# Optimization experiments

Hardware: AMD Instinct MI355X
Metric: run time of the kernel (lower is better)

Reference implementation:

```python
import jax, jax.numpy as jnp
import numpy as np

B, S, E, H, DH, F = 4, 2048, 1024, 4, 256, 4096


def setup_inputs() -> dict:
    key = jax.random.key(0)
    ks = jax.random.split(key, 16)
    def w(k, shape):
        return jax.random.normal(k, shape, jnp.float32) * 0.02
    return {
        "inputs": jax.random.normal(ks[0], (B, S, E), jnp.float32),
        "context": jax.random.normal(ks[1], (B, S, E), jnp.float32),
        # self-attention (causal) per-head projections stacked over heads
        "Wk1": w(ks[2], (H, E, DH)), "bk1": jnp.zeros((H, DH), jnp.float32),
        "Wq1": w(ks[3], (H, E, DH)), "bq1": jnp.zeros((H, DH), jnp.float32),
        "Wv1": w(ks[4], (H, E, DH)), "bv1": jnp.zeros((H, DH), jnp.float32),
        "Wo1": w(ks[5], (E, E)), "bo1": jnp.zeros((E,), jnp.float32),
        # cross-attention (no mask)
        "Wk2": w(ks[6], (H, E, DH)), "bk2": jnp.zeros((H, DH), jnp.float32),
        "Wq2": w(ks[7], (H, E, DH)), "bq2": jnp.zeros((H, DH), jnp.float32),
        "Wv2": w(ks[8], (H, E, DH)), "bv2": jnp.zeros((H, DH), jnp.float32),
        "Wo2": w(ks[9], (E, E)), "bo2": jnp.zeros((E,), jnp.float32),
        "ln_g": jnp.ones((E,), jnp.float32), "ln_b": jnp.zeros((E,), jnp.float32),
        # FFN
        "W1": w(ks[10], (E, F)), "b1": jnp.zeros((F,), jnp.float32),
        "W2": w(ks[11], (F, E)), "b2": jnp.zeros((E,), jnp.float32),
    }


def _mha(kin, vin, qin, Wk, bk, Wq, bq, Wv, bv, Wo, bo, causal):
    # per-head Dense projections, batched over heads: [B,S,E] x [H,E,DH] -> [B,H,S,DH]
    K = jnp.einsum('bse,hed->bhsd', kin, Wk) + bk[None, :, None, :]
    Q = jnp.einsum('bse,hed->bhsd', qin, Wq) + bq[None, :, None, :]
    V = jnp.einsum('bse,hed->bhsd', vin, Wv) + bv[None, :, None, :]
    # NOTE: original divides by head_dim (K.get_shape()[2]), NOT sqrt(head_dim)
    scores = jnp.einsum('bhqd,bhkd->bhqk', Q, K) / K.shape[-1]
    if causal:
        sq, sk = scores.shape[-2], scores.shape[-1]
        mask = jnp.triu(jnp.full((sq, sk), -jnp.inf, scores.dtype), k=1)
        scores = scores + mask  # additive -inf strictly above the diagonal
    A = jax.nn.softmax(scores, axis=-1)
    # concat heads in order along the feature axis, then output Dense
    out = jnp.einsum('bhqk,bhkd->bqhd', A, V).reshape(qin.shape[0], qin.shape[1], -1)
    return out @ Wo + bo


def _ln(x, g, b):
    # keras LayerNormalization default epsilon = 1e-3
    m = x.mean(-1, keepdims=True)
    v = ((x - m) ** 2).mean(-1, keepdims=True)
    return (x - m) / jnp.sqrt(v + 1e-3) * g + b


def reference(inputs, context, Wk1, bk1, Wq1, bq1, Wv1, bv1, Wo1, bo1,
              Wk2, bk2, Wq2, bq2, Wv2, bv2, Wo2, bo2,
              ln_g, ln_b, W1, b1, W2, b2):
    # dropout layers are identity at inference
    a = _mha(inputs, inputs, inputs, Wk1, bk1, Wq1, bq1, Wv1, bv1, Wo1, bo1, True) + inputs
    a = _ln(a, ln_g, ln_b)
    # cross-attention: keys/values = context, queries = normalized self-attn output
    c = _mha(context, context, a, Wk2, bk2, Wq2, bq2, Wv2, bv2, Wo2, bo2, False) + a
    c = _ln(c, ln_g, ln_b)
    h = jax.nn.relu(c @ W1 + b1) @ W2 + b2 + c
    return jax.nn.relu(_ln(h, ln_g, ln_b))
```

## Files before the change

kernel.cpp:

```cpp
#include <hip/hip_runtime.h>

#define DEV __device__ __forceinline__

typedef unsigned short u16;
typedef __bf16 bf16x8 __attribute__((ext_vector_type(8)));
typedef bf16x8 __attribute__((may_alias)) bf16x8a;
typedef float f32x4 __attribute__((ext_vector_type(4)));
typedef float f32x16 __attribute__((ext_vector_type(16)));

constexpr int NB = 4, NS = 2048, NE = 1024, NH = 4, NDH = 256, NF = 4096;
constexpr int NR = NB * NS;

DEV u16 f2bf(float f) {
  unsigned u = __float_as_uint(f);
  u += 0x7fff + ((u >> 16) & 1);
  return (u16)(u >> 16);
}

DEV f32x4 mfma16(bf16x8 a, bf16x8 b, f32x4 c) {
  return __builtin_amdgcn_mfma_f32_16x16x32_bf16(a, b, c, 0, 0, 0);
}
DEV f32x16 mfma32(bf16x8 a, bf16x8 b, f32x16 c) {
  return __builtin_amdgcn_mfma_f32_32x32x16_bf16(a, b, c, 0, 0, 0);
}

DEV bf16x8 ldfrag(const u16* p) { return *(const bf16x8a*)p; }

DEV void gload_lds16(const void* g, void* l) {
  __builtin_amdgcn_global_load_lds(
      (const __attribute__((address_space(1))) void*)g,
      (__attribute__((address_space(3))) void*)l, 16, 0, 0);
}

DEV void blockbar() {
  asm volatile("" ::: "memory");
  __builtin_amdgcn_s_barrier();
  asm volatile("" ::: "memory");
}

DEV unsigned packbf(float a, float b) {
  union { __bf16 h[2]; unsigned u; } x;
  x.h[0] = (__bf16)a; x.h[1] = (__bf16)b;
  return x.u;
}

__global__ void cast_f32_bf16(const float* __restrict__ in, u16* __restrict__ out, int n4) {
  int i = blockIdx.x * 256 + threadIdx.x;
  if (i >= n4) return;
  float4 v = ((const float4*)in)[i];
  ushort4 o;
  o.x = f2bf(v.x); o.y = f2bf(v.y); o.z = f2bf(v.z); o.w = f2bf(v.w);
  ((ushort4*)out)[i] = o;
}

__global__ void transpose_cast(const float* __restrict__ in, u16* __restrict__ out, int R, int C) {
  __shared__ float t[32][33];
  size_t base = (size_t)blockIdx.z * R * C;
  int c0 = blockIdx.x * 32, r0 = blockIdx.y * 32;
  int x = threadIdx.x;
  for (int yy = threadIdx.y; yy < 32; yy += 8)
    t[yy][x] = in[base + (size_t)(r0 + yy) * C + c0 + x];
  __syncthreads();
  for (int yy = threadIdx.y; yy < 32; yy += 8)
    out[base + (size_t)(c0 + yy) * R + r0 + x] = f2bf(t[x][yy]);
}

__global__ void transpose_v(const u16* __restrict__ V, int vstride, u16* __restrict__ Vt) {
  __shared__ u16 t[32][34];
  int bh = blockIdx.z, b = bh >> 2, h = bh & (NH - 1);
  int s0 = blockIdx.x * 32, d0 = blockIdx.y * 32;
  int x = threadIdx.x;
  for (int yy = threadIdx.y; yy < 32; yy += 8)
    t[yy][x] = V[(size_t)(b * NS + s0 + yy) * vstride + h * NDH + d0 + x];
  __syncthreads();
  for (int yy = threadIdx.y; yy < 32; yy += 8)
    Vt[((size_t)bh * NDH + d0 + yy) * NS + s0 + x] = t[x][yy];
}

__global__ void copy_f32(const float* __restrict__ s, float* __restrict__ d, int n) {
  int i = blockIdx.x * 256 + threadIdx.x;
  if (i < n) d[i] = s[i];
}

template<int BN, int OUTF32, int RELU>
__global__ __launch_bounds__(512, 1)
void gemm8p(const u16* __restrict__ A, const u16* __restrict__ Bt,
            const float* __restrict__ bias, const float* __restrict__ res,
            float* __restrict__ outF, u16* __restrict__ outB,
            int M, int N, int K)
{
  constexpr int NFRAG = BN / 64;
  __shared__ __align__(16) u16 smem[32768 + 2 * BN * 64];

  int tid = threadIdx.x, w = tid >> 6, lane = tid & 63;
  int lr = lane & 15, lk = lane >> 4;
  int wm = w >> 2, wn = w & 3;

  int flat = blockIdx.y * gridDim.x + blockIdx.x;
  int cpx = (gridDim.x * gridDim.y) >> 3;
  int swz = (flat & 7) * cpx + (flat >> 3);
  int bx = swz % gridDim.x, by = swz / gridDim.x;
  int rowBlk = by * 256, colBlk = bx * BN;

  f32x4 acc[8][NFRAG];
#pragma unroll
  for (int f = 0; f < 8; f++)
#pragma unroll
    for (int n = 0; n < NFRAG; n++) acc[f][n] = (f32x4){0.f, 0.f, 0.f, 0.f};

  int srow = lane >> 3;
  int scol = ((lane & 7) ^ (srow & 7)) * 8;

  const u16* gA = A + (size_t)rowBlk * K;
  const u16* gB = Bt + (size_t)colBlk * K;

  auto stageA = [&](int t, int p, int h) {
#pragma unroll
    for (int j = 0; j < 2; j++) {
      int rbase = h * 128 + (w * 2 + j) * 8;
      gload_lds16(gA + (size_t)(rbase + srow) * K + t * 64 + scol,
                  &smem[(p * 256 + rbase) * 64]);
    }
  };
  auto stageB = [&](int t, int p, int h) {
#pragma unroll
    for (int j = 0; j < 2; j++) {
      int rbase = h * 128 + (w * 2 + j) * 8;
      gload_lds16(gB + (size_t)(rbase + srow) * K + t * 64 + scol,
                  &smem[32768 + (p * BN + rbase) * 64]);
    }
  };

  stageB(0, 0, 0);
  if (BN == 256) stageB(0, 0, 1);
  stageA(0, 0, 0);
  stageA(0, 0, 1);
  asm volatile("s_waitcnt vmcnt(0)" ::: "memory");
  blockbar();

  int NT = K >> 6;
  for (int t = 0; t < NT; t++) {
    int p = t & 1;
    bool pre = (t + 1 < NT);
    bf16x8 bf[NFRAG][2];
#pragma unroll
    for (int q = 0; q < 4; q++) {
      if (q == 0) {
#pragma unroll
        for (int n = 0; n < NFRAG; n++)
#pragma unroll
          for (int s = 0; s < 2; s++) {
            int rowB = wn * (BN >> 2) + n * 16 + lr;
            bf[n][s] = ldfrag(&smem[32768 + (p * BN + rowB) * 64 +
                                    (((s * 4 + lk) ^ (lr & 7)) * 8)]);
          }
      }
      bf16x8 af[2][2];
#pragma unroll
      for (int i = 0; i < 2; i++)
#pragma unroll
        for (int s = 0; s < 2; s++) {
          int rowA = wm * 128 + (q * 2 + i) * 16 + lr;
          af[i][s] = ldfrag(&smem[(p * 256 + rowA) * 64 +
                                  (((s * 4 + lk) ^ (lr & 7)) * 8)]);
        }
      if (pre) {
        if (BN == 256) {
          if (q == 0) { stageB(t + 1, p ^ 1, 0); stageB(t + 1, p ^ 1, 1); }
          else if (q == 1) stageA(t + 1, p ^ 1, 0);
          else if (q == 2) stageA(t + 1, p ^ 1, 1);
        } else {
          if (q == 0) stageB(t + 1, p ^ 1, 0);
          else if (q == 1) stageA(t + 1, p ^ 1, 0);
          else if (q == 2) stageA(t + 1, p ^ 1, 1);
        }
      }
      blockbar();
      asm volatile("s_waitcnt lgkmcnt(0)" ::: "memory");
      __builtin_amdgcn_s_setprio(1);
#pragma unroll
      for (int i = 0; i < 2; i++)
#pragma unroll
        for (int n = 0; n < NFRAG; n++)
#pragma unroll
          for (int s = 0; s < 2; s++)
            acc[q * 2 + i][n] = mfma16(af[i][s], bf[n][s], acc[q * 2 + i][n]);
      __builtin_amdgcn_s_setprio(0);
      if (q == 3) asm volatile("s_waitcnt vmcnt(0)" ::: "memory");
      blockbar();
    }
  }

  int orow0 = rowBlk + wm * 128;
  int ocol0 = colBlk + wn * (BN >> 2);
#pragma unroll
  for (int n = 0; n < NFRAG; n++) {
    int c = ocol0 + n * 16 + lr;
    float bv = bias[c];
#pragma unroll
    for (int f = 0; f < 8; f++) {
      int r0 = orow0 + f * 16 + lk * 4;
#pragma unroll
      for (int j = 0; j < 4; j++) {
        float v = acc[f][n][j] + bv;
        if (OUTF32) v += res[(size_t)(r0 + j) * N + c];
        if (RELU) v = fmaxf(v, 0.f);
        if (OUTF32) outF[(size_t)(r0 + j) * N + c] = v;
        else        outB[(size_t)(r0 + j) * N + c] = f2bf(v);
      }
    }
  }
}

template<int CAUSAL>
__global__ __launch_bounds__(512, 2)
void attn8w(const u16* __restrict__ Qp, int qstride,
            const u16* __restrict__ Kp, int kstride,
            const u16* __restrict__ Vt, u16* __restrict__ O)
{
  __shared__ __align__(16) u16 smem[65536];

  int bidx = blockIdx.x;
  int bh = bidx & 15;
  int qt = CAUSAL ? (15 - (bidx >> 4)) : (bidx >> 4);
  int b = bh >> 2, h = bh & 3;
  int tid = threadIdx.x, w = tid >> 6, lane = tid & 63;
  int L = lane & 31, hi = lane >> 5;
  int g = w >> 1, ks = w & 1;

  int qbase = qt * 128 + g * 32;

  const u16* qrow = Qp + (size_t)(b * NS + qbase + L) * qstride + h * NDH;
  bf16x8 qf[16];
#pragma unroll
  for (int s = 0; s < 16; s++) qf[s] = ldfrag(qrow + s * 16 + hi * 8);

  f32x16 oacc[8];
#pragma unroll
  for (int db = 0; db < 8; db++) oacc[db] = (f32x16){};
  float m = -1e30f, l = 0.f;

  int nkt = CAUSAL ? (2 * qt + 2) : (NS / 64);
  constexpr float SC = 1.0f / NDH;

  const u16* kbase = Kp + (size_t)(b * NS) * kstride + h * NDH;
  const u16* vbase = Vt + (size_t)bh * NDH * NS;

  auto stage = [&](int kt, int buf) {
#pragma unroll
    for (int ii = 0; ii < 4; ii++) {
      int gi = w * 4 + ii;
      int krow = 2 * gi + hi;
      int kcol = L ^ (krow & 31);
      gload_lds16(kbase + (size_t)(kt * 64 + krow) * kstride + kcol * 8,
                  &smem[buf * 16384 + gi * 512]);
      int vd = gi * 8 + (lane >> 3);
      int vg = (lane & 7) ^ (vd & 7);
      gload_lds16(vbase + (size_t)vd * NS + kt * 64 + vg * 8,
                  &smem[32768 + buf * 16384 + gi * 512]);
    }
  };

  stage(0, 0);

  for (int kt = 0; kt < nkt; kt++) {
    int buf = kt & 1;
    const u16* bK = &smem[buf * 16384];
    const u16* bV = &smem[32768 + buf * 16384];
    if (kt + 1 < nkt) {
      stage(kt + 1, buf ^ 1);
      asm volatile("s_waitcnt vmcnt(8)" ::: "memory");
    } else {
      asm volatile("s_waitcnt vmcnt(0)" ::: "memory");
    }
    blockbar();

    int ksub0 = kt * 64 + ks * 32;
    bool skip = CAUSAL && (ksub0 > qbase + 31);
    if (!skip) {
      bool domask = CAUSAL && (ksub0 + 31 > qbase);
      __builtin_amdgcn_s_setprio(1);
      f32x16 sa = (f32x16){};
#pragma unroll
      for (int s = 0; s < 16; s++) {
        int row = ks * 32 + L;
        bf16x8 kf = ldfrag(&bK[row * 256 + (((2 * s + hi) ^ L) & 31) * 8]);
        sa = mfma32(kf, qf[s], sa);
      }
      __builtin_amdgcn_s_setprio(0);

      float p[16];
      float tmax = -1e30f;
#pragma unroll
      for (int r = 0; r < 16; r++) {
        float v = sa[r] * SC;
        if (domask) {
          int key = ksub0 + (r & 3) + 8 * (r >> 2) + 4 * hi;
          if (key > qbase + L) v = -1e30f;
        }
        p[r] = v;
        tmax = fmaxf(tmax, v);
      }
      tmax = fmaxf(tmax, __shfl_xor(tmax, 32));

      float mn = m;
      if (!__all(tmax - m <= 5.0f)) {
        mn = fmaxf(m, tmax);
        float rs = __expf(m - mn);
        m = mn;
        l *= rs;
#pragma unroll
        for (int db = 0; db < 8; db++)
#pragma unroll
          for (int r = 0; r < 16; r++) oacc[db][r] *= rs;
      }
      float psum = 0.f;
#pragma unroll
      for (int r = 0; r < 16; r++) {
        p[r] = __expf(p[r] - mn);
        psum += p[r];
      }
      psum += __shfl_xor(psum, 32);
      l += psum;

      unsigned pk01 = packbf(p[0], p[1]),  pk23 = packbf(p[2], p[3]);
      unsigned pk45 = packbf(p[4], p[5]),  pk67 = packbf(p[6], p[7]);
      unsigned pk89 = packbf(p[8], p[9]),  pkab = packbf(p[10], p[11]);
      unsigned pkcd = packbf(p[12], p[13]), pkef = packbf(p[14], p[15]);
      unsigned s45 = (unsigned)__shfl_xor((int)pk45, 32);
      unsigned s67 = (unsigned)__shfl_xor((int)pk67, 32);
      unsigned s01 = (unsigned)__shfl_xor((int)pk01, 32);
      unsigned s23 = (unsigned)__shfl_xor((int)pk23, 32);
      unsigned scd = (unsigned)__shfl_xor((int)pkcd, 32);
      unsigned sef = (unsigned)__shfl_xor((int)pkef, 32);
      unsigned s89 = (unsigned)__shfl_xor((int)pk89, 32);
      unsigned sab = (unsigned)__shfl_xor((int)pkab, 32);
      union { unsigned u[4]; bf16x8 v; } fb0, fb1;
      fb0.u[0] = hi ? s45 : pk01;
      fb0.u[1] = hi ? s67 : pk23;
      fb0.u[2] = hi ? pk45 : s01;
      fb0.u[3] = hi ? pk67 : s23;
      fb1.u[0] = hi ? scd : pk89;
      fb1.u[1] = hi ? sef : pkab;
      fb1.u[2] = hi ? pkcd : s89;
      fb1.u[3] = hi ? pkef : sab;
      bf16x8 pb0 = fb0.v, pb1 = fb1.v;

      __builtin_amdgcn_s_setprio(1);
#pragma unroll
      for (int db = 0; db < 8; db++) {
        int vd = db * 32 + L;
        bf16x8 vf0 = ldfrag(&bV[vd * 64 + (((ks * 4 + hi) ^ (vd & 7)) & 7) * 8]);
        bf16x8 vf1 = ldfrag(&bV[vd * 64 + (((ks * 4 + 2 + hi) ^ (vd & 7)) & 7) * 8]);
        oacc[db] = mfma32(vf0, pb0, oacc[db]);
        oacc[db] = mfma32(vf1, pb1, oacc[db]);
      }
      __builtin_amdgcn_s_setprio(0);
    }
    blockbar();
  }

  float* fsm = (float*)smem;
  blockbar();
  if (hi == 0) { fsm[w * 64 + L * 2] = m; fsm[w * 64 + L * 2 + 1] = l; }
  blockbar();
  float mb = fsm[(w ^ 1) * 64 + L * 2];
  float lb = fsm[(w ^ 1) * 64 + L * 2 + 1];
  float M = fmaxf(m, mb);
  float eo = __expf(m - M);
  float lt = l * eo + lb * __expf(mb - M);
  blockbar();
  float* reg = fsm + g * 8192;
  if (w & 1) {
#pragma unroll
    for (int db = 0; db < 8; db++)
#pragma unroll
      for (int r = 0; r < 16; r++) {
        int d = db * 32 + (r & 3) + 8 * (r >> 2) + 4 * hi;
        reg[d * 32 + L] = oacc[db][r] * eo;
      }
  }
  blockbar();
  if (!(w & 1)) {
    float inv = 1.f / lt;
    size_t orow = (size_t)(b * NS + qbase + L) * NE + h * NDH;
#pragma unroll
    for (int db = 0; db < 8; db++) {
#pragma unroll
      for (int rq = 0; rq < 4; rq++) {
        int d0 = db * 32 + rq * 8 + hi * 4;
        float a0 = (oacc[db][rq * 4 + 0] * eo + reg[(d0 + 0) * 32 + L]) * inv;
        float a1 = (oacc[db][rq * 4 + 1] * eo + reg[(d0 + 1) * 32 + L]) * inv;
        float a2 = (oacc[db][rq * 4 + 2] * eo + reg[(d0 + 2) * 32 + L]) * inv;
        float a3 = (oacc[db][rq * 4 + 3] * eo + reg[(d0 + 3) * 32 + L]) * inv;
        uint2 wv;
        wv.x = packbf(a0, a1);
        wv.y = packbf(a2, a3);
        *(uint2*)&O[orow + d0] = wv;
      }
    }
  }
}

template<int RELU, int WBF>
__global__ __launch_bounds__(256)
void ln_kernel(const float* __restrict__ x, const float* __restrict__ g,
               const float* __restrict__ bb, float* __restrict__ outF,
               u16* __restrict__ outB)
{
  int row = blockIdx.x, tid = threadIdx.x;
  float4 v = ((const float4*)(x + (size_t)row * NE))[tid];
  float s = v.x + v.y + v.z + v.w;
  float s2 = v.x * v.x + v.y * v.y + v.z * v.z + v.w * v.w;
#pragma unroll
  for (int off = 32; off; off >>= 1) {
    s += __shfl_xor(s, off);
    s2 += __shfl_xor(s2, off);
  }
  __shared__ float red[8];
  int wid = tid >> 6, lane = tid & 63;
  if (lane == 0) { red[wid] = s; red[4 + wid] = s2; }
  __syncthreads();
  s = red[0] + red[1] + red[2] + red[3];
  s2 = red[4] + red[5] + red[6] + red[7];
  float mean = s * (1.f / NE);
  float var = s2 * (1.f / NE) - mean * mean;
  float rstd = rsqrtf(var + 1e-3f);
  float4 gg = ((const float4*)g)[tid];
  float4 bv = ((const float4*)bb)[tid];
  float4 o;
  o.x = (v.x - mean) * rstd * gg.x + bv.x;
  o.y = (v.y - mean) * rstd * gg.y + bv.y;
  o.z = (v.z - mean) * rstd * gg.z + bv.z;
  o.w = (v.w - mean) * rstd * gg.w + bv.w;
  if (RELU) {
    o.x = fmaxf(o.x, 0.f); o.y = fmaxf(o.y, 0.f);
    o.z = fmaxf(o.z, 0.f); o.w = fmaxf(o.w, 0.f);
  }
  ((float4*)(outF + (size_t)row * NE))[tid] = o;
  if (WBF) {
    ushort4 ob;
    ob.x = f2bf(o.x); ob.y = f2bf(o.y); ob.z = f2bf(o.z); ob.w = f2bf(o.w);
    ((ushort4*)(outB + (size_t)row * NE))[tid] = ob;
  }
}

constexpr size_t OFF_X    = 0;
constexpr size_t OFF_W    = OFF_X + 16777216;
constexpr size_t OFF_BIAS = OFF_W + 33554432;
constexpr size_t OFF_QKV  = OFF_BIAS + 32768;
constexpr size_t OFF_VT   = OFF_QKV + 50331648;
constexpr size_t OFF_T0   = OFF_VT + 16777216;
constexpr size_t OFF_A    = OFF_T0 + 33554432;
constexpr size_t OFF_ABF  = OFF_A + 33554432;

extern "C" void kernel_launch(void* const* d_in, const int* in_sizes, int n_in,
                              void* d_out, int out_size, void* d_ws, size_t ws_size,
                              hipStream_t stream) {
  (void)in_sizes; (void)n_in; (void)out_size; (void)ws_size;
  const float* inp = (const float*)d_in[0];
  const float* ctx = (const float*)d_in[1];
  const float* Wk1 = (const float*)d_in[2];  const float* bk1 = (const float*)d_in[3];
  const float* Wq1 = (const float*)d_in[4];  const float* bq1 = (const float*)d_in[5];
  const float* Wv1 = (const float*)d_in[6];  const float* bv1 = (const float*)d_in[7];
  const float* Wo1 = (const float*)d_in[8];  const float* bo1 = (const float*)d_in[9];
  const float* Wk2 = (const float*)d_in[10]; const float* bk2 = (const float*)d_in[11];
  const float* Wq2 = (const float*)d_in[12]; const float* bq2 = (const float*)d_in[13];
  const float* Wv2 = (const float*)d_in[14]; const float* bv2 = (const float*)d_in[15];
  const float* Wo2 = (const float*)d_in[16]; const float* bo2 = (const float*)d_in[17];
  const float* lng = (const float*)d_in[18]; const float* lnb = (const float*)d_in[19];
  const float* W1  = (const float*)d_in[20]; const float* b1  = (const float*)d_in[21];
  const float* W2  = (const float*)d_in[22]; const float* b2  = (const float*)d_in[23];
  float* out = (float*)d_out;
  char* ws = (char*)d_ws;

  u16* XBF    = (u16*)(ws + OFF_X);
  u16* WQKV1T = (u16*)(ws + OFF_W);
  u16* WKV2T  = WQKV1T + 3072 * 1024;
  u16* WQ2T   = WKV2T + 2048 * 1024;
  u16* WO1T   = WQ2T + 1024 * 1024;
  u16* WO2T   = WO1T + 1024 * 1024;
  u16* W1T    = WO2T + 1024 * 1024;
  u16* W2T    = W1T + 4096 * 1024;
  float* BQKV1 = (float*)(ws + OFF_BIAS);
  float* BKV2  = BQKV1 + 3072;
  u16* QKV  = (u16*)(ws + OFF_QKV);
  u16* Q2   = QKV + 8192 * 2048;
  u16* VT   = (u16*)(ws + OFF_VT);
  u16* MID  = QKV;
  float* T0 = (float*)(ws + OFF_T0);
  float* Af = (float*)(ws + OFF_A);
  u16* ABF  = (u16*)(ws + OFF_ABF);
  u16* Obuf = XBF;

  dim3 tb(32, 8);

  cast_f32_bf16<<<8192, 256, 0, stream>>>(inp, XBF, NR * NE / 4);
  transpose_cast<<<dim3(8, 32, 4), tb, 0, stream>>>(Wk1, WQKV1T,               NE, NDH);
  transpose_cast<<<dim3(8, 32, 4), tb, 0, stream>>>(Wq1, WQKV1T + 1024 * 1024, NE, NDH);
  transpose_cast<<<dim3(8, 32, 4), tb, 0, stream>>>(Wv1, WQKV1T + 2048 * 1024, NE, NDH);
  transpose_cast<<<dim3(32, 32, 1), tb, 0, stream>>>(Wo1, WO1T, NE, NE);
  transpose_cast<<<dim3(8, 32, 4), tb, 0, stream>>>(Wk2, WKV2T,               NE, NDH);
  transpose_cast<<<dim3(8, 32, 4), tb, 0, stream>>>(Wv2, WKV2T + 1024 * 1024, NE, NDH);
  transpose_cast<<<dim3(8, 32, 4), tb, 0, stream>>>(Wq2, WQ2T, NE, NDH);
  transpose_cast<<<dim3(32, 32, 1), tb, 0, stream>>>(Wo2, WO2T, NE, NE);
  transpose_cast<<<dim3(128, 32, 1), tb, 0, stream>>>(W1, W1T, NE, NF);
  transpose_cast<<<dim3(32, 128, 1), tb, 0, stream>>>(W2, W2T, NF, NE);
  copy_f32<<<4, 256, 0, stream>>>(bk1, BQKV1, 1024);
  copy_f32<<<4, 256, 0, stream>>>(bq1, BQKV1 + 1024, 1024);
  copy_f32<<<4, 256, 0, stream>>>(bv1, BQKV1 + 2048, 1024);
  copy_f32<<<4, 256, 0, stream>>>(bk2, BKV2, 1024);
  copy_f32<<<4, 256, 0, stream>>>(bv2, BKV2 + 1024, 1024);

  gemm8p<256, 0, 0><<<dim3(12, 32), 512, 0, stream>>>(XBF, WQKV1T, BQKV1, nullptr,
                                                      nullptr, QKV, NR, 3072, NE);
  transpose_v<<<dim3(64, 8, 16), tb, 0, stream>>>(QKV + 2048, 3072, VT);
  attn8w<1><<<256, 512, 0, stream>>>(QKV + 1024, 3072, QKV, 3072, VT, Obuf);
  gemm8p<128, 1, 0><<<dim3(8, 32), 512, 0, stream>>>(Obuf, WO1T, bo1, inp,
                                                     T0, nullptr, NR, NE, NE);
  ln_kernel<0, 1><<<NR, 256, 0, stream>>>(T0, lng, lnb, Af, ABF);

  cast_f32_bf16<<<8192, 256, 0, stream>>>(ctx, XBF, NR * NE / 4);
  gemm8p<256, 0, 0><<<dim3(8, 32), 512, 0, stream>>>(XBF, WKV2T, BKV2, nullptr,
                                                     nullptr, QKV, NR, 2048, NE);
  gemm8p<128, 0, 0><<<dim3(8, 32), 512, 0, stream>>>(ABF, WQ2T, bq2, nullptr,
                                                     nullptr, Q2, NR, NE, NE);
  transpose_v<<<dim3(64, 8, 16), tb, 0, stream>>>(QKV + 1024, 2048, VT);
  attn8w<0><<<256, 512, 0, stream>>>(Q2, 1024, QKV, 2048, VT, Obuf);
  gemm8p<128, 1, 0><<<dim3(8, 32), 512, 0, stream>>>(Obuf, WO2T, bo2, Af,
                                                     T0, nullptr, NR, NE, NE);
  ln_kernel<0, 1><<<NR, 256, 0, stream>>>(T0, lng, lnb, Af, ABF);

  gemm8p<256, 0, 1><<<dim3(16, 32), 512, 0, stream>>>(ABF, W1T, b1, nullptr,
                                                      nullptr, MID, NR, NF, NE);
  gemm8p<128, 1, 0><<<dim3(8, 32), 512, 0, stream>>>(MID, W2T, b2, Af,
                                                     T0, nullptr, NR, NE, NF);
  ln_kernel<1, 0><<<NR, 256, 0, stream>>>(T0, lng, lnb, out, nullptr);
}
```

Measured before the change: 744.9 us.

## Replace double-buffered GEMM mainloop with 4-stage K=32 ring buffer pipeline

The GEMM mainloop now uses a four-slot ring of K=32 half-tiles instead of two K=64 buffers. Loads run three stages ahead, and partial vmcnt waits let later loads stay in flight while the current stage computes. The LDS layout packs two rows per 64-element line with an XOR swizzle. This cuts the per-quarter barriers and exposed global-load latency, but it adds address arithmetic and needs correct vmcnt counts for each BN variant.

```diff
diff --git a/kernel.cpp b/kernel.cpp
--- a/kernel.cpp
+++ b/kernel.cpp
@@ -84,13 +84,15 @@
 
 template<int BN, int OUTF32, int RELU>
 __global__ __launch_bounds__(512, 1)
-void gemm8p(const u16* __restrict__ A, const u16* __restrict__ Bt,
+void gemm4r(const u16* __restrict__ A, const u16* __restrict__ Bt,
             const float* __restrict__ bias, const float* __restrict__ res,
             float* __restrict__ outF, u16* __restrict__ outB,
             int M, int N, int K)
 {
   constexpr int NFRAG = BN / 64;
-  __shared__ __align__(16) u16 smem[32768 + 2 * BN * 64];
+  constexpr int BREG = BN * 32;
+  constexpr int SPH = 2 + (BN == 256 ? 2 : 1);
+  __shared__ __align__(16) u16 smem[32768 + 4 * BREG];
 
   int tid = threadIdx.x, w = tid >> 6, lane = tid & 63;
   int lr = lane & 15, lk = lane >> 4;
@@ -108,87 +110,80 @@
 #pragma unroll
     for (int n = 0; n < NFRAG; n++) acc[f][n] = (f32x4){0.f, 0.f, 0.f, 0.f};
 
-  int srow = lane >> 3;
-  int scol = ((lane & 7) ^ (srow & 7)) * 8;
-
   const u16* gA = A + (size_t)rowBlk * K;
   const u16* gB = Bt + (size_t)colBlk * K;
 
-  auto stageA = [&](int t, int p, int h) {
+  int Rl = lane >> 3, sl = lane & 7;
+
+  auto stage = [&](int hs) {
+    int reg = hs & 3;
+    int k0 = hs * 32;
 #pragma unroll
     for (int j = 0; j < 2; j++) {
-      int rbase = h * 128 + (w * 2 + j) * 8;
-      gload_lds16(gA + (size_t)(rbase + srow) * K + t * 64 + scol,
-                  &smem[(p * 256 + rbase) * 64]);
+      int Rbase = j * 64 + w * 8;
+      int R = Rbase + Rl;
+      int p = sl ^ (R & 7);
+      int r = 2 * R + (p >> 2), g = p & 3;
+      gload_lds16(gA + (size_t)r * K + k0 + g * 8,
+                  &smem[reg * 8192 + Rbase * 64]);
+    }
+#pragma unroll
+    for (int j = 0; j < (BN == 256 ? 2 : 1); j++) {
+      int Rbase = j * 64 + w * 8;
+      int R = Rbase + Rl;
+      int p = sl ^ (R & 7);
+      int r = 2 * R + (p >> 2), g = p & 3;
+      gload_lds16(gB + (size_t)r * K + k0 + g * 8,
+                  &smem[32768 + reg * BREG + Rbase * 64]);
     }
   };
-  auto stageB = [&](int t, int p, int h) {
-#pragma unroll
-    for (int j = 0; j < 2; j++) {
-      int rbase = h * 128 + (w * 2 + j) * 8;
-      gload_lds16(gB + (size_t)(rbase + srow) * K + t * 64 + scol,
-                  &smem[32768 + (p * BN + rbase) * 64]);
-    }
-  };
-
-  stageB(0, 0, 0);
-  if (BN == 256) stageB(0, 0, 1);
-  stageA(0, 0, 0);
-  stageA(0, 0, 1);
-  asm volatile("s_waitcnt vmcnt(0)" ::: "memory");
-  blockbar();
-
-  int NT = K >> 6;
-  for (int t = 0; t < NT; t++) {
-    int p = t & 1;
-    bool pre = (t + 1 < NT);
-    bf16x8 bf[NFRAG][2];
-#pragma unroll
-    for (int q = 0; q < 4; q++) {
-      if (q == 0) {
-#pragma unroll
-        for (int n = 0; n < NFRAG; n++)
-#pragma unroll
-          for (int s = 0; s < 2; s++) {
-            int rowB = wn * (BN >> 2) + n * 16 + lr;
-            bf[n][s] = ldfrag(&smem[32768 + (p * BN + rowB) * 64 +
-                                    (((s * 4 + lk) ^ (lr & 7)) * 8)]);
-          }
-      }
-      bf16x8 af[2][2];
-#pragma unroll
-      for (int i = 0; i < 2; i++)
-#pragma unroll
-        for (int s = 0; s < 2; s++) {
-          int rowA = wm * 128 + (q * 2 + i) * 16 + lr;
-          af[i][s] = ldfrag(&smem[(p * 256 + rowA) * 64 +
-                                  (((s * 4 + lk) ^ (lr & 7)) * 8)]);
-        }
-      if (pre) {
-        if (BN == 256) {
-          if (q == 0) { stageB(t + 1, p ^ 1, 0); stageB(t + 1, p ^ 1, 1); }
-          else if (q == 1) stageA(t + 1, p ^ 1, 0);
-          else if (q == 2) stageA(t + 1, p ^ 1, 1);
-        } else {
-          if (q == 0) stageB(t + 1, p ^ 1, 0);
-          else if (q == 1) stageA(t + 1, p ^ 1, 0);
-          else if (q == 2) stageA(t + 1, p ^ 1, 1);
-        }
-      }
-      blockbar();
-      asm volatile("s_waitcnt lgkmcnt(0)" ::: "memory");
-      __builtin_amdgcn_s_setprio(1);
-#pragma unroll
-      for (int i = 0; i < 2; i++)
-#pragma unroll
-        for (int n = 0; n < NFRAG; n++)
-#pragma unroll
-          for (int s = 0; s < 2; s++)
-            acc[q * 2 + i][n] = mfma16(af[i][s], bf[n][s], acc[q * 2 + i][n]);
-      __builtin_amdgcn_s_setprio(0);
-      if (q == 3) asm volatile("s_waitcnt vmcnt(0)" ::: "memory");
-      blockbar();
-    }
+
+  int NH32 = K >> 5;
+  stage(0); stage(1); stage(2);
+
+  for (int hs = 0; hs < NH32; hs++) {
+    if (hs + 3 < NH32) stage(hs + 3);
+    int rem = NH32 - 1 - hs;
+    if (rem > 3) rem = 3;
+    if (BN == 256) {
+      if (rem == 3)      asm volatile("s_waitcnt vmcnt(12)" ::: "memory");
+      else if (rem == 2) asm volatile("s_waitcnt vmcnt(8)" ::: "memory");
+      else if (rem == 1) asm volatile("s_waitcnt vmcnt(4)" ::: "memory");
+      else               asm volatile("s_waitcnt vmcnt(0)" ::: "memory");
+    } else {
+      if (rem == 3)      asm volatile("s_waitcnt vmcnt(9)" ::: "memory");
+      else if (rem == 2) asm volatile("s_waitcnt vmcnt(6)" ::: "memory");
+      else if (rem == 1) asm volatile("s_waitcnt vmcnt(3)" ::: "memory");
+      else               asm volatile("s_waitcnt vmcnt(0)" ::: "memory");
+    }
+    blockbar();
+
+    int reg = hs & 3;
+    const u16* Ar = &smem[reg * 8192];
+    const u16* Br = &smem[32768 + reg * BREG];
+    bf16x8 af[8], bfr[NFRAG];
+#pragma unroll
+    for (int f = 0; f < 8; f++) {
+      int rowA = wm * 128 + f * 16 + lr;
+      af[f] = ldfrag(&Ar[(rowA >> 1) * 64 +
+                         (((((rowA & 1) << 2) | lk) ^ ((rowA >> 1) & 7)) * 8)]);
+    }
+#pragma unroll
+    for (int n = 0; n < NFRAG; n++) {
+      int rowB = wn * (BN >> 2) + n * 16 + lr;
+      bfr[n] = ldfrag(&Br[(rowB >> 1) * 64 +
+                          (((((rowB & 1) << 2) | lk) ^ ((rowB >> 1) & 7)) * 8)]);
+    }
+    asm volatile("s_waitcnt lgkmcnt(0)" ::: "memory");
+    blockbar();
+
+    __builtin_amdgcn_s_setprio(1);
+#pragma unroll
+    for (int f = 0; f < 8; f++)
+#pragma unroll
+      for (int n = 0; n < NFRAG; n++)
+        acc[f][n] = mfma16(af[f], bfr[n], acc[f][n]);
+    __builtin_amdgcn_s_setprio(0);
   }
 
   int orow0 = rowBlk + wm * 128;
@@ -512,28 +507,28 @@
   copy_f32<<<4, 256, 0, stream>>>(bk2, BKV2, 1024);
   copy_f32<<<4, 256, 0, stream>>>(bv2, BKV2 + 1024, 1024);
 
-  gemm8p<256, 0, 0><<<dim3(12, 32), 512, 0, stream>>>(XBF, WQKV1T, BQKV1, nullptr,
+  gemm4r<256, 0, 0><<<dim3(12, 32), 512, 0, stream>>>(XBF, WQKV1T, BQKV1, nullptr,
                                                       nullptr, QKV, NR, 3072, NE);
   transpose_v<<<dim3(64, 8, 16), tb, 0, stream>>>(QKV + 2048, 3072, VT);
   attn8w<1><<<256, 512, 0, stream>>>(QKV + 1024, 3072, QKV, 3072, VT, Obuf);
-  gemm8p<128, 1, 0><<<dim3(8, 32), 512, 0, stream>>>(Obuf, WO1T, bo1, inp,
+  gemm4r<128, 1, 0><<<dim3(8, 32), 512, 0, stream>>>(Obuf, WO1T, bo1, inp,
                                                      T0, nullptr, NR, NE, NE);
   ln_kernel<0, 1><<<NR, 256, 0, stream>>>(T0, lng, lnb, Af, ABF);
 
   cast_f32_bf16<<<8192, 256, 0, stream>>>(ctx, XBF, NR * NE / 4);
-  gemm8p<256, 0, 0><<<dim3(8, 32), 512, 0, stream>>>(XBF, WKV2T, BKV2, nullptr,
+  gemm4r<256, 0, 0><<<dim3(8, 32), 512, 0, stream>>>(XBF, WKV2T, BKV2, nullptr,
                                                      nullptr, QKV, NR, 2048, NE);
-  gemm8p<128, 0, 0><<<dim3(8, 32), 512, 0, stream>>>(ABF, WQ2T, bq2, nullptr,
+  gemm4r<128, 0, 0><<<dim3(8, 32), 512, 0, stream>>>(ABF, WQ2T, bq2, nullptr,
                                                      nullptr, Q2, NR, NE, NE);
   transpose_v<<<dim3(64, 8, 16), tb, 0, stream>>>(QKV + 1024, 2048, VT);
   attn8w<0><<<256, 512, 0, stream>>>(Q2, 1024, QKV, 2048, VT, Obuf);
-  gemm8p<128, 1, 0><<<dim3(8, 32), 512, 0, stream>>>(Obuf, WO2T, bo2, Af,
+  gemm4r<128, 1, 0><<<dim3(8, 32), 512, 0, stream>>>(Obuf, WO2T, bo2, Af,
                                                      T0, nullptr, NR, NE, NE);
   ln_kernel<0, 1><<<NR, 256, 0, stream>>>(T0, lng, lnb, Af, ABF);
 
-  gemm8p<256, 0, 1><<<dim3(16, 32), 512, 0, stream>>>(ABF, W1T, b1, nullptr,
+  gemm4r<256, 0, 1><<<dim3(16, 32), 512, 0, stream>>>(ABF, W1T, b1, nullptr,
                                                       nullptr, MID, NR, NF, NE);
-  gemm8p<128, 1, 0><<<dim3(8, 32), 512, 0, stream>>>(MID, W2T, b2, Af,
+  gemm4r<128, 1, 0><<<dim3(8, 32), 512, 0, stream>>>(MID, W2T, b2, Af,
                                                      T0, nullptr, NR, NE, NF);
   ln_kernel<1, 0><<<NR, 256, 0, stream>>>(T0, lng, lnb, out, nullptr);
 }
```

Result: no change. 755.6 us (+1.4%).

## Halve attention block size and split K/V staging into a single-buffered pipeline

Applied to the files above, without the earlier changes.

Replaces the 8-wave, 128-query attention block with a 4-wave, 64-query block launched as 512 blocks, and halves shared memory by dropping K/V double buffering. The next K tile is now loaded during softmax and the next V tile after the PV product, with extra barriers between phases. The goal is more blocks for the 256 CUs and lower LDS use per block, so occupancy and causal load balance improve. The cost is more barriers per key tile and less load overlap than the old double-buffered scheme.

```diff
diff --git a/kernel.cpp b/kernel.cpp
--- a/kernel.cpp
+++ b/kernel.cpp
@@ -213,22 +213,22 @@
 }
 
 template<int CAUSAL>
-__global__ __launch_bounds__(512, 2)
-void attn8w(const u16* __restrict__ Qp, int qstride,
+__global__ __launch_bounds__(256, 2)
+void attn4w(const u16* __restrict__ Qp, int qstride,
             const u16* __restrict__ Kp, int kstride,
             const u16* __restrict__ Vt, u16* __restrict__ O)
 {
-  __shared__ __align__(16) u16 smem[65536];
+  __shared__ __align__(16) u16 smem[32768];
 
   int bidx = blockIdx.x;
   int bh = bidx & 15;
-  int qt = CAUSAL ? (15 - (bidx >> 4)) : (bidx >> 4);
+  int qt = CAUSAL ? (31 - (bidx >> 4)) : (bidx >> 4);
   int b = bh >> 2, h = bh & 3;
   int tid = threadIdx.x, w = tid >> 6, lane = tid & 63;
   int L = lane & 31, hi = lane >> 5;
   int g = w >> 1, ks = w & 1;
 
-  int qbase = qt * 128 + g * 32;
+  int qbase = qt * 64 + g * 32;
 
   const u16* qrow = Qp + (size_t)(b * NS + qbase + L) * qstride + h * NDH;
   bf16x8 qf[16];
@@ -240,55 +240,61 @@
   for (int db = 0; db < 8; db++) oacc[db] = (f32x16){};
   float m = -1e30f, l = 0.f;
 
-  int nkt = CAUSAL ? (2 * qt + 2) : (NS / 64);
+  int nkt = CAUSAL ? (qt + 1) : (NS / 64);
   constexpr float SC = 1.0f / NDH;
 
   const u16* kbase = Kp + (size_t)(b * NS) * kstride + h * NDH;
   const u16* vbase = Vt + (size_t)bh * NDH * NS;
 
-  auto stage = [&](int kt, int buf) {
-#pragma unroll
-    for (int ii = 0; ii < 4; ii++) {
-      int gi = w * 4 + ii;
+  auto stageK = [&](int kt) {
+#pragma unroll
+    for (int ii = 0; ii < 8; ii++) {
+      int gi = w * 8 + ii;
       int krow = 2 * gi + hi;
       int kcol = L ^ (krow & 31);
       gload_lds16(kbase + (size_t)(kt * 64 + krow) * kstride + kcol * 8,
-                  &smem[buf * 16384 + gi * 512]);
+                  &smem[gi * 512]);
+    }
+  };
+  auto stageV = [&](int kt) {
+#pragma unroll
+    for (int ii = 0; ii < 8; ii++) {
+      int gi = w * 8 + ii;
       int vd = gi * 8 + (lane >> 3);
       int vg = (lane & 7) ^ (vd & 7);
       gload_lds16(vbase + (size_t)vd * NS + kt * 64 + vg * 8,
-                  &smem[32768 + buf * 16384 + gi * 512]);
+                  &smem[16384 + gi * 512]);
     }
   };
 
-  stage(0, 0);
+  stageK(0);
+  asm volatile("" ::: "memory");
+  stageV(0);
+  asm volatile("s_waitcnt vmcnt(0)" ::: "memory");
+  blockbar();
 
   for (int kt = 0; kt < nkt; kt++) {
-    int buf = kt & 1;
-    const u16* bK = &smem[buf * 16384];
-    const u16* bV = &smem[32768 + buf * 16384];
-    if (kt + 1 < nkt) {
-      stage(kt + 1, buf ^ 1);
-      asm volatile("s_waitcnt vmcnt(8)" ::: "memory");
-    } else {
-      asm volatile("s_waitcnt vmcnt(0)" ::: "memory");
-    }
-    blockbar();
-
+    bool last = (kt + 1 == nkt);
     int ksub0 = kt * 64 + ks * 32;
     bool skip = CAUSAL && (ksub0 > qbase + 31);
+    bool domask = CAUSAL && !skip && (ksub0 + 31 > qbase);
+
+    f32x16 sa = (f32x16){};
     if (!skip) {
-      bool domask = CAUSAL && (ksub0 + 31 > qbase);
       __builtin_amdgcn_s_setprio(1);
-      f32x16 sa = (f32x16){};
 #pragma unroll
       for (int s = 0; s < 16; s++) {
         int row = ks * 32 + L;
-        bf16x8 kf = ldfrag(&bK[row * 256 + (((2 * s + hi) ^ L) & 31) * 8]);
+        bf16x8 kf = ldfrag(&smem[row * 256 + (((2 * s + hi) ^ L) & 31) * 8]);
         sa = mfma32(kf, qf[s], sa);
       }
       __builtin_amdgcn_s_setprio(0);
-
+    }
+    blockbar();
+    if (!last) stageK(kt + 1);
+
+    bf16x8 pb0, pb1;
+    if (!skip) {
       float p[16];
       float tmax = -1e30f;
 #pragma unroll
@@ -344,31 +350,44 @@
       fb1.u[1] = hi ? sef : pkab;
       fb1.u[2] = hi ? pkcd : s89;
       fb1.u[3] = hi ? pkef : sab;
-      bf16x8 pb0 = fb0.v, pb1 = fb1.v;
-
+      pb0 = fb0.v; pb1 = fb1.v;
+    }
+
+    if (!last) asm volatile("s_waitcnt vmcnt(8)" ::: "memory");
+    else       asm volatile("s_waitcnt vmcnt(0)" ::: "memory");
+    blockbar();
+
+    if (!skip) {
       __builtin_amdgcn_s_setprio(1);
 #pragma unroll
       for (int db = 0; db < 8; db++) {
         int vd = db * 32 + L;
-        bf16x8 vf0 = ldfrag(&bV[vd * 64 + (((ks * 4 + hi) ^ (vd & 7)) & 7) * 8]);
-        bf16x8 vf1 = ldfrag(&bV[vd * 64 + (((ks * 4 + 2 + hi) ^ (vd & 7)) & 7) * 8]);
+        bf16x8 vf0 = ldfrag(&smem[16384 + vd * 64 + (((ks * 4 + hi) ^ (vd & 7)) & 7) * 8]);
+        bf16x8 vf1 = ldfrag(&smem[16384 + vd * 64 + (((ks * 4 + 2 + hi) ^ (vd & 7)) & 7) * 8]);
         oacc[db] = mfma32(vf0, pb0, oacc[db]);
         oacc[db] = mfma32(vf1, pb1, oacc[db]);
       }
       __builtin_amdgcn_s_setprio(0);
     }
     blockbar();
+    if (!last) {
+      stageV(kt + 1);
+      asm volatile("s_waitcnt vmcnt(8)" ::: "memory");
+      blockbar();
+    }
   }
 
   float* fsm = (float*)smem;
   blockbar();
   if (hi == 0) { fsm[w * 64 + L * 2] = m; fsm[w * 64 + L * 2 + 1] = l; }
+  asm volatile("s_waitcnt lgkmcnt(0)" ::: "memory");
   blockbar();
   float mb = fsm[(w ^ 1) * 64 + L * 2];
   float lb = fsm[(w ^ 1) * 64 + L * 2 + 1];
   float M = fmaxf(m, mb);
   float eo = __expf(m - M);
   float lt = l * eo + lb * __expf(mb - M);
+  asm volatile("s_waitcnt lgkmcnt(0)" ::: "memory");
   blockbar();
   float* reg = fsm + g * 8192;
   if (w & 1) {
@@ -380,6 +399,7 @@
         reg[d * 32 + L] = oacc[db][r] * eo;
       }
   }
+  asm volatile("s_waitcnt lgkmcnt(0)" ::: "memory");
   blockbar();
   if (!(w & 1)) {
     float inv = 1.f / lt;
@@ -515,7 +535,7 @@
   gemm8p<256, 0, 0><<<dim3(12, 32), 512, 0, stream>>>(XBF, WQKV1T, BQKV1, nullptr,
                                                       nullptr, QKV, NR, 3072, NE);
   transpose_v<<<dim3(64, 8, 16), tb, 0, stream>>>(QKV + 2048, 3072, VT);
-  attn8w<1><<<256, 512, 0, stream>>>(QKV + 1024, 3072, QKV, 3072, VT, Obuf);
+  attn4w<1><<<512, 256, 0, stream>>>(QKV + 1024, 3072, QKV, 3072, VT, Obuf);
   gemm8p<128, 1, 0><<<dim3(8, 32), 512, 0, stream>>>(Obuf, WO1T, bo1, inp,
                                                      T0, nullptr, NR, NE, NE);
   ln_kernel<0, 1><<<NR, 256, 0, stream>>>(T0, lng, lnb, Af, ABF);
@@ -526,7 +546,7 @@
   gemm8p<128, 0, 0><<<dim3(8, 32), 512, 0, stream>>>(ABF, WQ2T, bq2, nullptr,
                                                      nullptr, Q2, NR, NE, NE);
   transpose_v<<<dim3(64, 8, 16), tb, 0, stream>>>(QKV + 1024, 2048, VT);
-  attn8w<0><<<256, 512, 0, stream>>>(Q2, 1024, QKV, 2048, VT, Obuf);
+  attn4w<0><<<512, 256, 0, stream>>>(Q2, 1024, QKV, 2048, VT, Obuf);
   gemm8p<128, 1, 0><<<dim3(8, 32), 512, 0, stream>>>(Obuf, WO2T, bo2, Af,
                                                      T0, nullptr, NR, NE, NE);
   ln_kernel<0, 1><<<NR, 256, 0, stream>>>(T0, lng, lnb, Af, ABF);
```

Result: slower. 762.3 us (+2.3%).

## Split causal attention KV range across two blocks and merge partials

Applied to the files above, without the earlier changes.

The causal self-attention kernel now launches 512 blocks instead of 256, with each query tile's key range cut into two halves processed by separate blocks. Each block writes unnormalized fp32 partial outputs plus row max and sum, and a new merge kernel combines them with a log-sum-exp rescale and writes bf16. The aim is better occupancy and load balance on the many-CU GPU, since 256 blocks underfill it and causal tiles have uneven work. The cost is an extra kernel launch, fp32 partial traffic through reused workspace buffers, and some explicit LDS waitcnts added before barriers.

```diff
diff --git a/kernel.cpp b/kernel.cpp
--- a/kernel.cpp
+++ b/kernel.cpp
@@ -212,17 +212,31 @@
   }
 }
 
-template<int CAUSAL>
+template<int CAUSAL, int SPLIT>
 __global__ __launch_bounds__(512, 2)
 void attn8w(const u16* __restrict__ Qp, int qstride,
             const u16* __restrict__ Kp, int kstride,
-            const u16* __restrict__ Vt, u16* __restrict__ O)
+            const u16* __restrict__ Vt, u16* __restrict__ O,
+            float* __restrict__ Op, float* __restrict__ ml)
 {
   __shared__ __align__(16) u16 smem[65536];
 
   int bidx = blockIdx.x;
-  int bh = bidx & 15;
-  int qt = CAUSAL ? (15 - (bidx >> 4)) : (bidx >> 4);
+  int bh, qt, kt0, kt1;
+  if (SPLIT) {
+    int qtIdx = bidx >> 5;
+    qt = 15 - qtIdx;
+    int sub = bidx & 31;
+    int half = sub >> 4;
+    bh = sub & 15;
+    kt0 = half ? (qt + 1) : 0;
+    kt1 = half ? (2 * qt + 2) : (qt + 1);
+  } else {
+    bh = bidx & 15;
+    qt = CAUSAL ? (15 - (bidx >> 4)) : (bidx >> 4);
+    kt0 = 0;
+    kt1 = CAUSAL ? (2 * qt + 2) : (NS / 64);
+  }
   int b = bh >> 2, h = bh & 3;
   int tid = threadIdx.x, w = tid >> 6, lane = tid & 63;
   int L = lane & 31, hi = lane >> 5;
@@ -240,7 +254,6 @@
   for (int db = 0; db < 8; db++) oacc[db] = (f32x16){};
   float m = -1e30f, l = 0.f;
 
-  int nkt = CAUSAL ? (2 * qt + 2) : (NS / 64);
   constexpr float SC = 1.0f / NDH;
 
   const u16* kbase = Kp + (size_t)(b * NS) * kstride + h * NDH;
@@ -261,13 +274,14 @@
     }
   };
 
-  stage(0, 0);
-
-  for (int kt = 0; kt < nkt; kt++) {
-    int buf = kt & 1;
+  stage(kt0, 0);
+  asm volatile("" ::: "memory");
+
+  for (int kt = kt0; kt < kt1; kt++) {
+    int buf = (kt - kt0) & 1;
     const u16* bK = &smem[buf * 16384];
     const u16* bV = &smem[32768 + buf * 16384];
-    if (kt + 1 < nkt) {
+    if (kt + 1 < kt1) {
       stage(kt + 1, buf ^ 1);
       asm volatile("s_waitcnt vmcnt(8)" ::: "memory");
     } else {
@@ -363,12 +377,14 @@
   float* fsm = (float*)smem;
   blockbar();
   if (hi == 0) { fsm[w * 64 + L * 2] = m; fsm[w * 64 + L * 2 + 1] = l; }
+  asm volatile("s_waitcnt lgkmcnt(0)" ::: "memory");
   blockbar();
   float mb = fsm[(w ^ 1) * 64 + L * 2];
   float lb = fsm[(w ^ 1) * 64 + L * 2 + 1];
   float M = fmaxf(m, mb);
   float eo = __expf(m - M);
   float lt = l * eo + lb * __expf(mb - M);
+  asm volatile("s_waitcnt lgkmcnt(0)" ::: "memory");
   blockbar();
   float* reg = fsm + g * 8192;
   if (w & 1) {
@@ -380,25 +396,81 @@
         reg[d * 32 + L] = oacc[db][r] * eo;
       }
   }
+  asm volatile("s_waitcnt lgkmcnt(0)" ::: "memory");
   blockbar();
   if (!(w & 1)) {
-    float inv = 1.f / lt;
-    size_t orow = (size_t)(b * NS + qbase + L) * NE + h * NDH;
-#pragma unroll
-    for (int db = 0; db < 8; db++) {
-#pragma unroll
-      for (int rq = 0; rq < 4; rq++) {
-        int d0 = db * 32 + rq * 8 + hi * 4;
-        float a0 = (oacc[db][rq * 4 + 0] * eo + reg[(d0 + 0) * 32 + L]) * inv;
-        float a1 = (oacc[db][rq * 4 + 1] * eo + reg[(d0 + 1) * 32 + L]) * inv;
-        float a2 = (oacc[db][rq * 4 + 2] * eo + reg[(d0 + 2) * 32 + L]) * inv;
-        float a3 = (oacc[db][rq * 4 + 3] * eo + reg[(d0 + 3) * 32 + L]) * inv;
-        uint2 wv;
-        wv.x = packbf(a0, a1);
-        wv.y = packbf(a2, a3);
-        *(uint2*)&O[orow + d0] = wv;
-      }
-    }
+    if (SPLIT) {
+      float* OpB = Op + (size_t)bidx * 32768 + (size_t)(g * 32 + L) * 256;
+      if (hi == 0) {
+        ml[((size_t)bidx * 128 + g * 32 + L) * 2]     = M;
+        ml[((size_t)bidx * 128 + g * 32 + L) * 2 + 1] = lt;
+      }
+#pragma unroll
+      for (int db = 0; db < 8; db++) {
+#pragma unroll
+        for (int rq = 0; rq < 4; rq++) {
+          int d0 = db * 32 + rq * 8 + hi * 4;
+          float4 v;
+          v.x = oacc[db][rq * 4 + 0] * eo + reg[(d0 + 0) * 32 + L];
+          v.y = oacc[db][rq * 4 + 1] * eo + reg[(d0 + 1) * 32 + L];
+          v.z = oacc[db][rq * 4 + 2] * eo + reg[(d0 + 2) * 32 + L];
+          v.w = oacc[db][rq * 4 + 3] * eo + reg[(d0 + 3) * 32 + L];
+          *(float4*)(OpB + d0) = v;
+        }
+      }
+    } else {
+      float inv = 1.f / lt;
+      size_t orow = (size_t)(b * NS + qbase + L) * NE + h * NDH;
+#pragma unroll
+      for (int db = 0; db < 8; db++) {
+#pragma unroll
+        for (int rq = 0; rq < 4; rq++) {
+          int d0 = db * 32 + rq * 8 + hi * 4;
+          float a0 = (oacc[db][rq * 4 + 0] * eo + reg[(d0 + 0) * 32 + L]) * inv;
+          float a1 = (oacc[db][rq * 4 + 1] * eo + reg[(d0 + 1) * 32 + L]) * inv;
+          float a2 = (oacc[db][rq * 4 + 2] * eo + reg[(d0 + 2) * 32 + L]) * inv;
+          float a3 = (oacc[db][rq * 4 + 3] * eo + reg[(d0 + 3) * 32 + L]) * inv;
+          uint2 wv;
+          wv.x = packbf(a0, a1);
+          wv.y = packbf(a2, a3);
+          *(uint2*)&O[orow + d0] = wv;
+        }
+      }
+    }
+  }
+}
+
+__global__ __launch_bounds__(256)
+void merge_attn(const float* __restrict__ Op, const float* __restrict__ ml,
+                u16* __restrict__ O)
+{
+  int blk = blockIdx.x;
+  int qt = blk >> 4, bh = blk & 15;
+  int b = bh >> 2, h = bh & 3;
+  int p0 = (15 - qt) * 32 + bh;
+  int p1 = p0 + 16;
+  int tid = threadIdx.x;
+  int row = tid >> 1;
+  int dbase = (tid & 1) * 128;
+
+  float m0 = ml[((size_t)p0 * 128 + row) * 2];
+  float l0 = ml[((size_t)p0 * 128 + row) * 2 + 1];
+  float m1 = ml[((size_t)p1 * 128 + row) * 2];
+  float l1 = ml[((size_t)p1 * 128 + row) * 2 + 1];
+  float M = fmaxf(m0, m1);
+  float e0 = __expf(m0 - M), e1 = __expf(m1 - M);
+  float inv = 1.f / (l0 * e0 + l1 * e1);
+  const float* O0 = Op + ((size_t)p0 * 128 + row) * 256 + dbase;
+  const float* O1 = Op + ((size_t)p1 * 128 + row) * 256 + dbase;
+  u16* dst = O + (size_t)(b * NS + qt * 128 + row) * NE + h * NDH + dbase;
+#pragma unroll
+  for (int d = 0; d < 128; d += 4) {
+    float4 a = *(const float4*)(O0 + d);
+    float4 c = *(const float4*)(O1 + d);
+    uint2 wv;
+    wv.x = packbf((a.x * e0 + c.x * e1) * inv, (a.y * e0 + c.y * e1) * inv);
+    wv.y = packbf((a.z * e0 + c.z * e1) * inv, (a.w * e0 + c.w * e1) * inv);
+    *(uint2*)(dst + d) = wv;
   }
 }
 
@@ -489,8 +561,10 @@
   u16* VT   = (u16*)(ws + OFF_VT);
   u16* MID  = QKV;
   float* T0 = (float*)(ws + OFF_T0);
+  float* OpBuf = T0;
   float* Af = (float*)(ws + OFF_A);
   u16* ABF  = (u16*)(ws + OFF_ABF);
+  float* MlBuf = (float*)(ws + OFF_ABF);
   u16* Obuf = XBF;
 
   dim3 tb(32, 8);
@@ -515,7 +589,9 @@
   gemm8p<256, 0, 0><<<dim3(12, 32), 512, 0, stream>>>(XBF, WQKV1T, BQKV1, nullptr,
                                                       nullptr, QKV, NR, 3072, NE);
   transpose_v<<<dim3(64, 8, 16), tb, 0, stream>>>(QKV + 2048, 3072, VT);
-  attn8w<1><<<256, 512, 0, stream>>>(QKV + 1024, 3072, QKV, 3072, VT, Obuf);
+  attn8w<1, 1><<<512, 512, 0, stream>>>(QKV + 1024, 3072, QKV, 3072, VT,
+                                        nullptr, OpBuf, MlBuf);
+  merge_attn<<<256, 256, 0, stream>>>(OpBuf, MlBuf, Obuf);
   gemm8p<128, 1, 0><<<dim3(8, 32), 512, 0, stream>>>(Obuf, WO1T, bo1, inp,
                                                      T0, nullptr, NR, NE, NE);
   ln_kernel<0, 1><<<NR, 256, 0, stream>>>(T0, lng, lnb, Af, ABF);
@@ -526,7 +602,8 @@
   gemm8p<128, 0, 0><<<dim3(8, 32), 512, 0, stream>>>(ABF, WQ2T, bq2, nullptr,
                                                      nullptr, Q2, NR, NE, NE);
   transpose_v<<<dim3(64, 8, 16), tb, 0, stream>>>(QKV + 1024, 2048, VT);
-  attn8w<0><<<256, 512, 0, stream>>>(Q2, 1024, QKV, 2048, VT, Obuf);
+  attn8w<0, 0><<<256, 512, 0, stream>>>(Q2, 1024, QKV, 2048, VT, Obuf,
+                                        nullptr, nullptr);
   gemm8p<128, 1, 0><<<dim3(8, 32), 512, 0, stream>>>(Obuf, WO2T, bo2, Af,
                                                      T0, nullptr, NR, NE, NE);
   ln_kernel<0, 1><<<NR, 256, 0, stream>>>(T0, lng, lnb, Af, ABF);
```

Result: faster. 727.0 us (-2.4%).
